# Performance work log

Hardware: AMD Instinct MI355X
Metric: run time of the kernel (lower is better)

## Reference

```python
import jax, jax.numpy as jnp
import numpy as np

D = 64          # slot_dim == input_dim
K = 8           # num_slots
NUM_ITERS = 3
EPS = 1e-8      # attention renorm eps
LN_EPS = 1e-5   # torch LayerNorm default
SCALE = float(np.sqrt(D))


def _ln(x, g, b):
    m = x.mean(-1, keepdims=True)
    v = ((x - m) ** 2).mean(-1, keepdims=True)
    return (x - m) / jnp.sqrt(v + LN_EPS) * g + b


def setup_inputs() -> dict:
    key = jax.random.key(0)
    ks = jax.random.split(key, 12)
    B, N = 128, 4096
    s = 1.0 / np.sqrt(D)
    return {
        "inputs": jax.random.normal(ks[0], (B, N, D), jnp.float32),
        "noise": jax.random.normal(ks[1], (B, K, D), jnp.float32),
        "slot_mu": jax.random.normal(ks[2], (1, 1, D), jnp.float32),
        "slot_log_sigma": jnp.zeros((1, 1, D), jnp.float32),
        "Wq": jax.random.normal(ks[3], (D, D), jnp.float32) * s,
        "Wk": jax.random.normal(ks[4], (D, D), jnp.float32) * s,
        "Wv": jax.random.normal(ks[5], (D, D), jnp.float32) * s,
        "gru_wih": jax.random.normal(ks[6], (3 * D, D), jnp.float32) * s,
        "gru_whh": jax.random.normal(ks[7], (3 * D, D), jnp.float32) * s,
        "gru_bih": jnp.zeros((3 * D,), jnp.float32),
        "gru_bhh": jnp.zeros((3 * D,), jnp.float32),
        "ln_in_g": jnp.ones((D,), jnp.float32),
        "ln_in_b": jnp.zeros((D,), jnp.float32),
        "ln_s_g": jnp.ones((D,), jnp.float32),
        "ln_s_b": jnp.zeros((D,), jnp.float32),
        "mlp_ln_g": jnp.ones((D,), jnp.float32),
        "mlp_ln_b": jnp.zeros((D,), jnp.float32),
        "mlp_w1": jax.random.normal(ks[8], (4 * D, D), jnp.float32) * s,
        "mlp_b1": jnp.zeros((4 * D,), jnp.float32),
        "mlp_w2": jax.random.normal(ks[9], (D, 4 * D), jnp.float32) * (1.0 / np.sqrt(4 * D)),
        "mlp_b2": jnp.zeros((D,), jnp.float32),
    }


def reference(inputs, noise, slot_mu, slot_log_sigma, Wq, Wk, Wv,
              gru_wih, gru_whh, gru_bih, gru_bhh,
              ln_in_g, ln_in_b, ln_s_g, ln_s_b,
              mlp_ln_g, mlp_ln_b, mlp_w1, mlp_b1, mlp_w2, mlp_b2):
    x = _ln(inputs, ln_in_g, ln_in_b)          # (B, N, D)
    k = x @ Wk.T                               # (B, N, D)
    v = x @ Wv.T                               # (B, N, D)
    slots = slot_mu + jnp.exp(slot_log_sigma) * noise  # (B, K, D)
    for _ in range(NUM_ITERS):
        slots_prev = slots
        s = _ln(slots, ln_s_g, ln_s_b)
        q = s @ Wq.T                           # (B, K, D)
        attn = jnp.einsum('bkd,bnd->bkn', q, k) / SCALE
        attn = jax.nn.softmax(attn, axis=1)    # compete over slots
        attn_w = attn / (attn.sum(-1, keepdims=True) + EPS)
        updates = jnp.einsum('bkn,bnd->bkd', attn_w, v)
        # GRUCell(updates, slots_prev)
        gi = updates @ gru_wih.T + gru_bih
        gh = slots_prev @ gru_whh.T + gru_bhh
        i_r, i_z, i_n = jnp.split(gi, 3, axis=-1)
        h_r, h_z, h_n = jnp.split(gh, 3, axis=-1)
        r = jax.nn.sigmoid(i_r + h_r)
        z = jax.nn.sigmoid(i_z + h_z)
        n = jnp.tanh(i_n + r * h_n)
        slots = (1.0 - z) * n + z * slots_prev
        # residual MLP
        h = _ln(slots, mlp_ln_g, mlp_ln_b)
        slots = slots + jax.nn.relu(h @ mlp_w1.T + mlp_b1) @ mlp_w2.T + mlp_b2
    return slots
```

## Files before the change

### kernel.cpp

```cpp
#include <hip/hip_runtime.h>
#include <cstdint>

#define Bn 128
#define Nn 4096
#define Dn 64
#define Kn 8
#define PBn 8
#define NCHUNKn (Nn / PBn)
#define LN_EPSf 1e-5f
#define EPSf 1e-8f
#define LOG2Ef 1.4426950408889634f

typedef unsigned short u16x8 __attribute__((ext_vector_type(8)));

static __device__ __forceinline__ uint16_t f2bf(float f) {
    union { float f; uint32_t u; } v; v.f = f;
    return (uint16_t)((v.u + 0x7fffu + ((v.u >> 16) & 1u)) >> 16);
}
static __device__ __forceinline__ float bflo(uint32_t u) {
    union { uint32_t u; float f; } v; v.u = u << 16; return v.f;
}
static __device__ __forceinline__ float bfhi(uint32_t u) {
    union { uint32_t u; float f; } v; v.u = u & 0xffff0000u; return v.f;
}

template <int CTRL>
static __device__ __forceinline__ float dppadd(float x) {
    int p = __builtin_amdgcn_update_dpp(0, __float_as_int(x), CTRL, 0xf, 0xf, false);
    return x + __int_as_float(p);
}

__global__ __launch_bounds__(256) void kM(const float* __restrict__ Wq,
                                          const float* __restrict__ Wk,
                                          float* __restrict__ M) {
    const int idx = blockIdx.x * 256 + threadIdx.x;
    const int e = idx >> 6, f = idx & 63;
    float acc = 0.f;
#pragma unroll 8
    for (int d = 0; d < 64; ++d) acc += Wq[d * 64 + e] * Wk[d * 64 + f];
    M[idx] = acc * 0.125f * LOG2Ef;
}

__global__ __launch_bounds__(256) void kinit_qk_full(
    const float* __restrict__ noise, const float* __restrict__ mu,
    const float* __restrict__ ls, const float* __restrict__ M,
    const float* __restrict__ lsg, const float* __restrict__ lsb,
    float* __restrict__ slots, float* __restrict__ qk) {
    __shared__ float sraw[Kn * Dn];
    __shared__ float sln[Kn][68];
    const int t = threadIdx.x;
    const int b = blockIdx.x;

    if (t < 128) {
        const int base = (b * 128 + t) * 4;
        const int d = base & 63;
        float4 nz = *(const float4*)(noise + base);
        float4 m4 = *(const float4*)(mu + d);
        float4 s4 = *(const float4*)(ls + d);
        float4 o;
        o.x = m4.x + __expf(s4.x) * nz.x;
        o.y = m4.y + __expf(s4.y) * nz.y;
        o.z = m4.z + __expf(s4.z) * nz.z;
        o.w = m4.w + __expf(s4.w) * nz.w;
        *(float4*)(slots + base) = o;
        *(float4*)(sraw + t * 4) = o;
    }
    __syncthreads();
    if (t < 128) {
        const int row = t >> 4, l16 = t & 15;
        float4 v4 = *(const float4*)(sraw + row * 64 + l16 * 4);
        float s1 = v4.x + v4.y + v4.z + v4.w;
        float s2 = v4.x * v4.x + v4.y * v4.y + v4.z * v4.z + v4.w * v4.w;
        s1 = dppadd<0xB1>(s1); s2 = dppadd<0xB1>(s2);
        s1 = dppadd<0x4E>(s1); s2 = dppadd<0x4E>(s2);
        s1 = dppadd<0x141>(s1); s2 = dppadd<0x141>(s2);
        s1 = dppadd<0x128>(s1); s2 = dppadd<0x128>(s2);
        const float mean = s1 * (1.0f / 64.0f);
        const float var = s2 * (1.0f / 64.0f) - mean * mean;
        const float rstd = rsqrtf(var + LN_EPSf);
        const float xs[4] = {v4.x, v4.y, v4.z, v4.w};
#pragma unroll
        for (int i = 0; i < 4; ++i) {
            const int dcol = l16 * 4 + i;
            sln[row][dcol] = (xs[i] - mean) * rstd * lsg[dcol] + lsb[dcol];
        }
    }
    __syncthreads();
    for (int o = t; o < 512; o += 256) {
        const int kk = o >> 6, j = o & 63;
        float a = 0.f;
#pragma unroll 8
        for (int e = 0; e < 64; ++e) a += sln[kk][e] * M[e * 64 + j];
        qk[b * 512 + o] = a;
    }
}

template <int MODE>
__global__ __launch_bounds__(256) void k2_attn(
    const float* __restrict__ inp, const uint16_t* __restrict__ xbf_in,
    uint16_t* __restrict__ xbf_out, const float* __restrict__ qkg,
    const float* __restrict__ lng, const float* __restrict__ lnb,
    float* __restrict__ partials) {
    __shared__ float qld[Kn][64];
    __shared__ float red[16 * 552];
    __shared__ float redas[16][8];

    const int t = threadIdx.x;
    const int b = blockIdx.x >> 3;
    const int part = blockIdx.x & 7;

    if (t < 128) *(float4*)(&qld[0][0] + t * 4) = *(const float4*)(qkg + b * 512 + t * 4);
    __syncthreads();

    const int dc = t & 7;
    const int pg = t >> 3;
    float qr[8][8];
#pragma unroll
    for (int kk = 0; kk < 8; ++kk) {
        float4 q0 = *(const float4*)&qld[kk][dc * 8];
        float4 q1 = *(const float4*)&qld[kk][dc * 8 + 4];
        qr[kk][0] = q0.x; qr[kk][1] = q0.y; qr[kk][2] = q0.z; qr[kk][3] = q0.w;
        qr[kk][4] = q1.x; qr[kk][5] = q1.y; qr[kk][6] = q1.z; qr[kk][7] = q1.w;
    }

    float gv[8], bt[8];
    if (MODE == 0) {
#pragma unroll
        for (int i = 0; i < 8; ++i) { gv[i] = lng[dc * 8 + i]; bt[i] = lnb[dc * 8 + i]; }
    }

    float upd[8][8];
    float asum[8];
#pragma unroll
    for (int kk = 0; kk < 8; ++kk) {
        asum[kk] = 0.f;
#pragma unroll
        for (int i = 0; i < 8; ++i) upd[kk][i] = 0.f;
    }

    const long chunkoff = ((long)b * Nn + part * NCHUNKn) * 64 + dc * 8;
    const uint16_t* xbase = xbf_in + chunkoff;
    const float* ibase = inp + chunkoff;
    uint16_t* obase = xbf_out + chunkoff;

    uint4 xr;
    float4 fa, fb;
    if (MODE == 1) {
        xr = *(const uint4*)(xbase + (long)pg * 64);
    } else {
        fa = *(const float4*)(ibase + (long)pg * 64);
        fb = *(const float4*)(ibase + (long)pg * 64 + 4);
    }

    for (int it = 0; it < NCHUNKn / 32; ++it) {
        uint4 xn;
        float4 na, nb;
        if (it < NCHUNKn / 32 - 1) {
            if (MODE == 1) {
                xn = *(const uint4*)(xbase + (long)((it + 1) * 32 + pg) * 64);
            } else {
                na = *(const float4*)(ibase + (long)((it + 1) * 32 + pg) * 64);
                nb = *(const float4*)(ibase + (long)((it + 1) * 32 + pg) * 64 + 4);
            }
        } else {
            if (MODE == 1) xn = xr; else { na = fa; nb = fb; }
        }

        float xf[8];
        if (MODE == 1) {
            xf[0] = bflo(xr.x); xf[1] = bfhi(xr.x);
            xf[2] = bflo(xr.y); xf[3] = bfhi(xr.y);
            xf[4] = bflo(xr.z); xf[5] = bfhi(xr.z);
            xf[6] = bflo(xr.w); xf[7] = bfhi(xr.w);
        } else {
            float x8[8] = {fa.x, fa.y, fa.z, fa.w, fb.x, fb.y, fb.z, fb.w};
            float s1 = 0.f, s2 = 0.f;
#pragma unroll
            for (int i = 0; i < 8; ++i) { s1 += x8[i]; s2 += x8[i] * x8[i]; }
            s1 = dppadd<0xB1>(s1); s2 = dppadd<0xB1>(s2);
            s1 = dppadd<0x4E>(s1); s2 = dppadd<0x4E>(s2);
            s1 = dppadd<0x141>(s1); s2 = dppadd<0x141>(s2);
            const float mean = s1 * (1.0f / 64.0f);
            const float var = s2 * (1.0f / 64.0f) - mean * mean;
            const float rstd = rsqrtf(var + LN_EPSf);
#pragma unroll
            for (int i = 0; i < 8; ++i) xf[i] = (x8[i] - mean) * rstd * gv[i] + bt[i];
            u16x8 o;
#pragma unroll
            for (int i = 0; i < 8; ++i) o[i] = f2bf(xf[i]);
            *(u16x8*)(obase + (long)(it * 32 + pg) * 64) = o;
        }

        float lg[8];
#pragma unroll
        for (int kk = 0; kk < 8; ++kk) {
            float a = 0.f;
#pragma unroll
            for (int i = 0; i < 8; ++i) a += qr[kk][i] * xf[i];
            lg[kk] = a;
        }
#pragma unroll
        for (int kk = 0; kk < 8; ++kk) lg[kk] = dppadd<0xB1>(lg[kk]);
#pragma unroll
        for (int kk = 0; kk < 8; ++kk) lg[kk] = dppadd<0x4E>(lg[kk]);
#pragma unroll
        for (int kk = 0; kk < 8; ++kk) lg[kk] = dppadd<0x141>(lg[kk]);
        float e[8];
        float es = 0.f;
#pragma unroll
        for (int kk = 0; kk < 8; ++kk) { e[kk] = exp2f(lg[kk]); es += e[kk]; }
        const float rinv = __builtin_amdgcn_rcpf(es);
#pragma unroll
        for (int kk = 0; kk < 8; ++kk) {
            const float a = e[kk] * rinv;
            asum[kk] += a;
#pragma unroll
            for (int i = 0; i < 8; ++i) upd[kk][i] += a * xf[i];
        }
        if (MODE == 1) xr = xn; else { fa = na; fb = nb; }
    }

#pragma unroll
    for (int kk = 0; kk < 8; ++kk) {
#pragma unroll
        for (int i = 0; i < 8; ++i) upd[kk][i] = dppadd<0x128>(upd[kk][i]);
        asum[kk] = dppadd<0x128>(asum[kk]);
    }
    const int l = t & 63;
    const int wv = t >> 6;
    if ((l & 8) == 0) {
        const int copy = wv * 4 + (l >> 4);
        float* rb = red + copy * 552 + (l & 7) * 8;
#pragma unroll
        for (int kk = 0; kk < 8; ++kk) {
            float4 u0, u1;
            u0.x = upd[kk][0]; u0.y = upd[kk][1]; u0.z = upd[kk][2]; u0.w = upd[kk][3];
            u1.x = upd[kk][4]; u1.y = upd[kk][5]; u1.z = upd[kk][6]; u1.w = upd[kk][7];
            *(float4*)(rb + kk * 68) = u0;
            *(float4*)(rb + kk * 68 + 4) = u1;
        }
        if ((l & 15) == 0) {
            float4 a0, a1;
            a0.x = asum[0]; a0.y = asum[1]; a0.z = asum[2]; a0.w = asum[3];
            a1.x = asum[4]; a1.y = asum[5]; a1.z = asum[6]; a1.w = asum[7];
            *(float4*)&redas[copy][0] = a0;
            *(float4*)&redas[copy][4] = a1;
        }
    }
    __syncthreads();
    float* pout = partials + (long)(b * PBn + part) * 520;
    if (t < 128) {
        const int kk = t >> 4, dq = t & 15;
        float4 acc = {0.f, 0.f, 0.f, 0.f};
#pragma unroll
        for (int c = 0; c < 16; ++c) {
            float4 v = *(const float4*)(red + c * 552 + kk * 68 + dq * 4);
            acc.x += v.x; acc.y += v.y; acc.z += v.z; acc.w += v.w;
        }
        *(float4*)(pout + kk * 64 + dq * 4) = acc;
    }
    if (t < 8) {
        float a = 0.f;
#pragma unroll
        for (int c = 0; c < 16; ++c) a += redas[c][t];
        pout[512 + t] = a;
    }
}

__global__ __launch_bounds__(256) void k3_update(
    const float* __restrict__ partials, const float* __restrict__ slots_in,
    const float* __restrict__ Wv,
    const float* __restrict__ wih, const float* __restrict__ whh,
    const float* __restrict__ bih, const float* __restrict__ bhh,
    const float* __restrict__ mg, const float* __restrict__ mb,
    const float* __restrict__ w1, const float* __restrict__ b1,
    const float* __restrict__ w2, const float* __restrict__ b2,
    const float* __restrict__ M, const float* __restrict__ lsg,
    const float* __restrict__ lsb,
    float* __restrict__ slots_out, float* __restrict__ qkout) {
    __shared__ float axn[64];
    __shared__ float updf[64];
    __shared__ float sp[64];
    __shared__ float gi[192];
    __shared__ float gh[192];
    __shared__ float sn[64];
    __shared__ float hln[64];
    __shared__ float hid[256];
    __shared__ float outv[64];
    __shared__ float lnq[64];

    const int t = threadIdx.x;
    const int b = blockIdx.x >> 3;
    const int s = blockIdx.x & 7;
    const float* pp = partials + (long)b * PBn * 520;

    float asum = EPSf;
#pragma unroll
    for (int j = 0; j < PBn; ++j) asum += pp[j * 520 + 512 + s];
    const float rasum = 1.0f / asum;

    if (t < 64) {
        float a = 0.f;
#pragma unroll
        for (int j = 0; j < PBn; ++j) a += pp[j * 520 + s * 64 + t];
        axn[t] = a * rasum;
    } else if (t < 80) {
        const int i = t - 64;
        *(float4*)&sp[i * 4] = *(const float4*)(slots_in + b * 512 + s * 64 + i * 4);
    }
    __syncthreads();

    {
        const int d = t >> 2, h = t & 3;
        const float* wr = Wv + d * 64 + h * 16;
        float acc = 0.f;
#pragma unroll
        for (int u = 0; u < 4; ++u) {
            float4 w4 = *(const float4*)(wr + u * 4);
            float4 a4 = *(const float4*)&axn[h * 16 + u * 4];
            acc += w4.x * a4.x + w4.y * a4.y + w4.z * a4.z + w4.w * a4.w;
        }
        acc = dppadd<0xB1>(acc);
        acc = dppadd<0x4E>(acc);
        if (h == 0) updf[d] = acc;
    }
    __syncthreads();

    for (int w = t; w < 768; w += 256) {
        const int j = w >> 2, h = w & 3;
        const float* wr = wih + j * 64 + h * 16;
        float acc = 0.f;
#pragma unroll
        for (int u = 0; u < 4; ++u) {
            float4 w4 = *(const float4*)(wr + u * 4);
            float4 a4 = *(const float4*)&updf[h * 16 + u * 4];
            acc += w4.x * a4.x + w4.y * a4.y + w4.z * a4.z + w4.w * a4.w;
        }
        acc = dppadd<0xB1>(acc);
        acc = dppadd<0x4E>(acc);
        if (h == 0) gi[j] = acc + bih[j];
    }
    for (int w = t; w < 768; w += 256) {
        const int j = w >> 2, h = w & 3;
        const float* wr = whh + j * 64 + h * 16;
        float acc = 0.f;
#pragma unroll
        for (int u = 0; u < 4; ++u) {
            float4 w4 = *(const float4*)(wr + u * 4);
            float4 a4 = *(const float4*)&sp[h * 16 + u * 4];
            acc += w4.x * a4.x + w4.y * a4.y + w4.z * a4.z + w4.w * a4.w;
        }
        acc = dppadd<0xB1>(acc);
        acc = dppadd<0x4E>(acc);
        if (h == 0) gh[j] = acc + bhh[j];
    }
    __syncthreads();

    if (t < 64) {
        const float ir = gi[t], iz = gi[64 + t], in_ = gi[128 + t];
        const float hr = gh[t], hz = gh[64 + t], hn = gh[128 + t];
        const float r = 1.0f / (1.0f + __expf(-(ir + hr)));
        const float z = 1.0f / (1.0f + __expf(-(iz + hz)));
        const float n = tanhf(in_ + r * hn);
        sn[t] = (1.0f - z) * n + z * sp[t];
    }
    __syncthreads();

    if (t < 16) {
        float4 v4 = *(const float4*)&sn[t * 4];
        float s1 = v4.x + v4.y + v4.z + v4.w;
        float s2 = v4.x * v4.x + v4.y * v4.y + v4.z * v4.z + v4.w * v4.w;
        s1 = dppadd<0xB1>(s1); s2 = dppadd<0xB1>(s2);
        s1 = dppadd<0x4E>(s1); s2 = dppadd<0x4E>(s2);
        s1 = dppadd<0x141>(s1); s2 = dppadd<0x141>(s2);
        s1 = dppadd<0x128>(s1); s2 = dppadd<0x128>(s2);
        const float mean = s1 * (1.0f / 64.0f);
        const float var = s2 * (1.0f / 64.0f) - mean * mean;
        const float rstd = rsqrtf(var + LN_EPSf);
        const float xs[4] = {v4.x, v4.y, v4.z, v4.w};
#pragma unroll
        for (int i = 0; i < 4; ++i) {
            const int dcol = t * 4 + i;
            hln[dcol] = (xs[i] - mean) * rstd * mg[dcol] + mb[dcol];
        }
    }
    __syncthreads();

    for (int w = t; w < 1024; w += 256) {
        const int j = w >> 2, h = w & 3;
        const float* wr = w1 + j * 64 + h * 16;
        float acc = 0.f;
#pragma unroll
        for (int u = 0; u < 4; ++u) {
            float4 w4 = *(const float4*)(wr + u * 4);
            float4 a4 = *(const float4*)&hln[h * 16 + u * 4];
            acc += w4.x * a4.x + w4.y * a4.y + w4.z * a4.z + w4.w * a4.w;
        }
        acc = dppadd<0xB1>(acc);
        acc = dppadd<0x4E>(acc);
        if (h == 0) hid[j] = fmaxf(acc + b1[j], 0.0f);
    }
    __syncthreads();

    {
        const int d = t >> 2, h = t & 3;
        const float* wr = w2 + d * 256 + h * 64;
        float acc = 0.f;
#pragma unroll
        for (int u = 0; u < 16; ++u) {
            float4 w4 = *(const float4*)(wr + u * 4);
            float4 h4 = *(const float4*)&hid[h * 64 + u * 4];
            acc += w4.x * h4.x + w4.y * h4.y + w4.z * h4.z + w4.w * h4.w;
        }
        acc = dppadd<0xB1>(acc);
        acc = dppadd<0x4E>(acc);
        if (h == 0) {
            const float val = sn[d] + acc + b2[d];
            slots_out[(long)b * 512 + s * 64 + d] = val;
            outv[d] = val;
        }
    }
    __syncthreads();

    if (t < 16) {
        float4 v4 = *(const float4*)&outv[t * 4];
        float s1 = v4.x + v4.y + v4.z + v4.w;
        float s2 = v4.x * v4.x + v4.y * v4.y + v4.z * v4.z + v4.w * v4.w;
        s1 = dppadd<0xB1>(s1); s2 = dppadd<0xB1>(s2);
        s1 = dppadd<0x4E>(s1); s2 = dppadd<0x4E>(s2);
        s1 = dppadd<0x141>(s1); s2 = dppadd<0x141>(s2);
        s1 = dppadd<0x128>(s1); s2 = dppadd<0x128>(s2);
        const float mean = s1 * (1.0f / 64.0f);
        const float var = s2 * (1.0f / 64.0f) - mean * mean;
        const float rstd = rsqrtf(var + LN_EPSf);
        const float xs[4] = {v4.x, v4.y, v4.z, v4.w};
#pragma unroll
        for (int i = 0; i < 4; ++i) {
            const int dcol = t * 4 + i;
            lnq[dcol] = (xs[i] - mean) * rstd * lsg[dcol] + lsb[dcol];
        }
    }
    __syncthreads();
    if (t < 64) {
        float a = 0.f;
#pragma unroll 8
        for (int e = 0; e < 64; ++e) a += lnq[e] * M[e * 64 + t];
        qkout[b * 512 + s * 64 + t] = a;
    }
}

extern "C" void kernel_launch(void* const* d_in, const int* in_sizes, int n_in,
                              void* d_out, int out_size, void* d_ws, size_t ws_size,
                              hipStream_t stream) {
    const float* inputs = (const float*)d_in[0];
    const float* noise = (const float*)d_in[1];
    const float* mu = (const float*)d_in[2];
    const float* ls = (const float*)d_in[3];
    const float* Wq = (const float*)d_in[4];
    const float* Wk = (const float*)d_in[5];
    const float* Wv = (const float*)d_in[6];
    const float* wih = (const float*)d_in[7];
    const float* whh = (const float*)d_in[8];
    const float* bih = (const float*)d_in[9];
    const float* bhh = (const float*)d_in[10];
    const float* lng = (const float*)d_in[11];
    const float* lnb = (const float*)d_in[12];
    const float* lsg = (const float*)d_in[13];
    const float* lsb = (const float*)d_in[14];
    const float* mg = (const float*)d_in[15];
    const float* mb = (const float*)d_in[16];
    const float* w1 = (const float*)d_in[17];
    const float* b1 = (const float*)d_in[18];
    const float* w2 = (const float*)d_in[19];
    const float* b2 = (const float*)d_in[20];

    char* ws = (char*)d_ws;
    float* slots = (float*)ws;
    float* Mm = (float*)(ws + 262144);
    float* qk = (float*)(ws + 262144 + 16384);
    uint16_t* xbf = (uint16_t*)(ws + 262144 + 16384 + 262144);
    float* parts = (float*)(ws + 262144 + 16384 + 262144 + (1 << 26));

    kM<<<16, 256, 0, stream>>>(Wq, Wk, Mm);
    kinit_qk_full<<<Bn, 256, 0, stream>>>(noise, mu, ls, Mm, lsg, lsb, slots, qk);
    for (int it = 0; it < 3; ++it) {
        if (it == 0)
            k2_attn<0><<<Bn * PBn, 256, 0, stream>>>(inputs, xbf, xbf, qk, lng, lnb, parts);
        else
            k2_attn<1><<<Bn * PBn, 256, 0, stream>>>(inputs, xbf, xbf, qk, lng, lnb, parts);
        float* dst = (it == 2) ? (float*)d_out : slots;
        k3_update<<<Bn * Kn, 256, 0, stream>>>(parts, slots, Wv, wih, whh, bih, bhh,
                                               mg, mb, w1, b1, w2, b2, Mm, lsg, lsb,
                                               dst, qk);
    }
}
```

Before: 182.8 us.

## Use bf16 dot2 for attention logits and double-buffer loads in attention kernel

Computes the q·x logits with packed bf16 fdot2 instructions, using bf16-packed q values and the bf16 x values directly, which cuts the FMA count for the logit dot products. The main loop now keeps two chunks in flight with prefetch distance two to hide global load latency, and the launch bounds request 3 blocks per SM to limit register use. Rounding q to bf16 lowers logit precision slightly, and the extra prefetch registers may cause spills under the tighter register budget.

```diff
diff --git a/kernel.cpp b/kernel.cpp
--- a/kernel.cpp
+++ b/kernel.cpp
@@ -7,11 +7,22 @@
 #define Kn 8
 #define PBn 8
 #define NCHUNKn (Nn / PBn)
+#define NITn (NCHUNKn / 32)
 #define LN_EPSf 1e-5f
 #define EPSf 1e-8f
 #define LOG2Ef 1.4426950408889634f
 
 typedef unsigned short u16x8 __attribute__((ext_vector_type(8)));
+
+#if __has_builtin(__builtin_amdgcn_fdot2_f32_bf16)
+#define USE_DOT2 1
+typedef __bf16 bf16v2 __attribute__((ext_vector_type(2)));
+static __device__ __forceinline__ bf16v2 asbf2(uint32_t u) {
+    union { uint32_t u; bf16v2 v; } c; c.u = u; return c.v;
+}
+#else
+#define USE_DOT2 0
+#endif
 
 static __device__ __forceinline__ uint16_t f2bf(float f) {
     union { float f; uint32_t u; } v; v.f = f;
@@ -96,7 +107,7 @@
 }
 
 template <int MODE>
-__global__ __launch_bounds__(256) void k2_attn(
+__global__ __launch_bounds__(256, 3) void k2_attn(
     const float* __restrict__ inp, const uint16_t* __restrict__ xbf_in,
     uint16_t* __restrict__ xbf_out, const float* __restrict__ qkg,
     const float* __restrict__ lng, const float* __restrict__ lnb,
@@ -114,6 +125,16 @@
 
     const int dc = t & 7;
     const int pg = t >> 3;
+
+#if USE_DOT2
+    uint32_t qrp[8][4];
+#pragma unroll
+    for (int kk = 0; kk < 8; ++kk)
+#pragma unroll
+        for (int p = 0; p < 4; ++p)
+            qrp[kk][p] = (uint32_t)f2bf(qld[kk][dc * 8 + 2 * p]) |
+                         ((uint32_t)f2bf(qld[kk][dc * 8 + 2 * p + 1]) << 16);
+#else
     float qr[8][8];
 #pragma unroll
     for (int kk = 0; kk < 8; ++kk) {
@@ -122,6 +143,7 @@
         qr[kk][0] = q0.x; qr[kk][1] = q0.y; qr[kk][2] = q0.z; qr[kk][3] = q0.w;
         qr[kk][4] = q1.x; qr[kk][5] = q1.y; qr[kk][6] = q1.z; qr[kk][7] = q1.w;
     }
+#endif
 
     float gv[8], bt[8];
     if (MODE == 0) {
@@ -139,66 +161,32 @@
     }
 
     const long chunkoff = ((long)b * Nn + part * NCHUNKn) * 64 + dc * 8;
-    const uint16_t* xbase = xbf_in + chunkoff;
-    const float* ibase = inp + chunkoff;
-    uint16_t* obase = xbf_out + chunkoff;
-
-    uint4 xr;
-    float4 fa, fb;
-    if (MODE == 1) {
-        xr = *(const uint4*)(xbase + (long)pg * 64);
-    } else {
-        fa = *(const float4*)(ibase + (long)pg * 64);
-        fb = *(const float4*)(ibase + (long)pg * 64 + 4);
-    }
-
-    for (int it = 0; it < NCHUNKn / 32; ++it) {
-        uint4 xn;
-        float4 na, nb;
-        if (it < NCHUNKn / 32 - 1) {
-            if (MODE == 1) {
-                xn = *(const uint4*)(xbase + (long)((it + 1) * 32 + pg) * 64);
-            } else {
-                na = *(const float4*)(ibase + (long)((it + 1) * 32 + pg) * 64);
-                nb = *(const float4*)(ibase + (long)((it + 1) * 32 + pg) * 64 + 4);
-            }
-        } else {
-            if (MODE == 1) xn = xr; else { na = fa; nb = fb; }
-        }
-
-        float xf[8];
-        if (MODE == 1) {
-            xf[0] = bflo(xr.x); xf[1] = bfhi(xr.x);
-            xf[2] = bflo(xr.y); xf[3] = bfhi(xr.y);
-            xf[4] = bflo(xr.z); xf[5] = bfhi(xr.z);
-            xf[6] = bflo(xr.w); xf[7] = bfhi(xr.w);
-        } else {
-            float x8[8] = {fa.x, fa.y, fa.z, fa.w, fb.x, fb.y, fb.z, fb.w};
-            float s1 = 0.f, s2 = 0.f;
-#pragma unroll
-            for (int i = 0; i < 8; ++i) { s1 += x8[i]; s2 += x8[i] * x8[i]; }
-            s1 = dppadd<0xB1>(s1); s2 = dppadd<0xB1>(s2);
-            s1 = dppadd<0x4E>(s1); s2 = dppadd<0x4E>(s2);
-            s1 = dppadd<0x141>(s1); s2 = dppadd<0x141>(s2);
-            const float mean = s1 * (1.0f / 64.0f);
-            const float var = s2 * (1.0f / 64.0f) - mean * mean;
-            const float rstd = rsqrtf(var + LN_EPSf);
-#pragma unroll
-            for (int i = 0; i < 8; ++i) xf[i] = (x8[i] - mean) * rstd * gv[i] + bt[i];
-            u16x8 o;
-#pragma unroll
-            for (int i = 0; i < 8; ++i) o[i] = f2bf(xf[i]);
-            *(u16x8*)(obase + (long)(it * 32 + pg) * 64) = o;
-        }
-
+    const uint16_t* xbase = xbf_in + chunkoff + (long)pg * 64;
+    const float* ibase = inp + chunkoff + (long)pg * 64;
+    uint16_t* obase = xbf_out + chunkoff + (long)pg * 64;
+
+    auto attend = [&](const uint32_t px0, const uint32_t px1, const uint32_t px2,
+                      const uint32_t px3, const float* xf) {
         float lg[8];
+#if USE_DOT2
 #pragma unroll
         for (int kk = 0; kk < 8; ++kk) {
             float a = 0.f;
+            a = __builtin_amdgcn_fdot2_f32_bf16(asbf2(qrp[kk][0]), asbf2(px0), a, false);
+            a = __builtin_amdgcn_fdot2_f32_bf16(asbf2(qrp[kk][1]), asbf2(px1), a, false);
+            a = __builtin_amdgcn_fdot2_f32_bf16(asbf2(qrp[kk][2]), asbf2(px2), a, false);
+            a = __builtin_amdgcn_fdot2_f32_bf16(asbf2(qrp[kk][3]), asbf2(px3), a, false);
+            lg[kk] = a;
+        }
+#else
+#pragma unroll
+        for (int kk = 0; kk < 8; ++kk) {
+            float a = 0.f;
 #pragma unroll
             for (int i = 0; i < 8; ++i) a += qr[kk][i] * xf[i];
             lg[kk] = a;
         }
+#endif
 #pragma unroll
         for (int kk = 0; kk < 8; ++kk) lg[kk] = dppadd<0xB1>(lg[kk]);
 #pragma unroll
@@ -206,9 +194,9 @@
 #pragma unroll
         for (int kk = 0; kk < 8; ++kk) lg[kk] = dppadd<0x141>(lg[kk]);
         float e[8];
-        float es = 0.f;
-#pragma unroll
-        for (int kk = 0; kk < 8; ++kk) { e[kk] = exp2f(lg[kk]); es += e[kk]; }
+#pragma unroll
+        for (int kk = 0; kk < 8; ++kk) e[kk] = exp2f(lg[kk]);
+        const float es = ((e[0] + e[1]) + (e[2] + e[3])) + ((e[4] + e[5]) + (e[6] + e[7]));
         const float rinv = __builtin_amdgcn_rcpf(es);
 #pragma unroll
         for (int kk = 0; kk < 8; ++kk) {
@@ -217,7 +205,71 @@
 #pragma unroll
             for (int i = 0; i < 8; ++i) upd[kk][i] += a * xf[i];
         }
-        if (MODE == 1) xr = xn; else { fa = na; fb = nb; }
+    };
+
+    auto body1 = [&](const uint4 x4) {
+        float xf[8];
+        xf[0] = bflo(x4.x); xf[1] = bfhi(x4.x);
+        xf[2] = bflo(x4.y); xf[3] = bfhi(x4.y);
+        xf[4] = bflo(x4.z); xf[5] = bfhi(x4.z);
+        xf[6] = bflo(x4.w); xf[7] = bfhi(x4.w);
+        attend(x4.x, x4.y, x4.z, x4.w, xf);
+    };
+
+    auto body0 = [&](const float4 fa, const float4 fb, const int pos) {
+        float x8[8] = {fa.x, fa.y, fa.z, fa.w, fb.x, fb.y, fb.z, fb.w};
+        float s1 = 0.f, s2 = 0.f;
+#pragma unroll
+        for (int i = 0; i < 8; ++i) { s1 += x8[i]; s2 += x8[i] * x8[i]; }
+        s1 = dppadd<0xB1>(s1); s2 = dppadd<0xB1>(s2);
+        s1 = dppadd<0x4E>(s1); s2 = dppadd<0x4E>(s2);
+        s1 = dppadd<0x141>(s1); s2 = dppadd<0x141>(s2);
+        const float mean = s1 * (1.0f / 64.0f);
+        const float var = s2 * (1.0f / 64.0f) - mean * mean;
+        const float rstd = rsqrtf(var + LN_EPSf);
+        float xf[8];
+        u16x8 o;
+#pragma unroll
+        for (int i = 0; i < 8; ++i) {
+            xf[i] = (x8[i] - mean) * rstd * gv[i] + bt[i];
+            o[i] = f2bf(xf[i]);
+        }
+        *(u16x8*)(obase + (long)pos * 2048) = o;
+        const uint32_t p0 = (uint32_t)o[0] | ((uint32_t)o[1] << 16);
+        const uint32_t p1 = (uint32_t)o[2] | ((uint32_t)o[3] << 16);
+        const uint32_t p2 = (uint32_t)o[4] | ((uint32_t)o[5] << 16);
+        const uint32_t p3 = (uint32_t)o[6] | ((uint32_t)o[7] << 16);
+        attend(p0, p1, p2, p3, xf);
+    };
+
+    if (MODE == 1) {
+        uint4 xrA = *(const uint4*)(xbase);
+        uint4 xrB = *(const uint4*)(xbase + 2048);
+        int it = 0;
+        for (; it < NITn - 2; it += 2) {
+            uint4 nA = *(const uint4*)(xbase + (long)(it + 2) * 2048);
+            body1(xrA); xrA = nA;
+            uint4 nB = *(const uint4*)(xbase + (long)(it + 3) * 2048);
+            body1(xrB); xrB = nB;
+        }
+        body1(xrA);
+        body1(xrB);
+    } else {
+        float4 faA = *(const float4*)(ibase);
+        float4 fbA = *(const float4*)(ibase + 4);
+        float4 faB = *(const float4*)(ibase + 2048);
+        float4 fbB = *(const float4*)(ibase + 2048 + 4);
+        int it = 0;
+        for (; it < NITn - 2; it += 2) {
+            float4 nA0 = *(const float4*)(ibase + (long)(it + 2) * 2048);
+            float4 nA1 = *(const float4*)(ibase + (long)(it + 2) * 2048 + 4);
+            body0(faA, fbA, it); faA = nA0; fbA = nA1;
+            float4 nB0 = *(const float4*)(ibase + (long)(it + 3) * 2048);
+            float4 nB1 = *(const float4*)(ibase + (long)(it + 3) * 2048 + 4);
+            body0(faB, fbB, it + 1); faB = nB0; fbB = nB1;
+        }
+        body0(faA, fbA, NITn - 2);
+        body0(faB, fbB, NITn - 1);
     }
 
 #pragma unroll
```

Result: faster. 172.7 us (-5.5%).
